# Kernel optimization log

Measured on AMD Instinct MI355X. Metric: run time of the kernel, lower is better.

## Reference

```python
import jax, jax.numpy as jnp
import numpy as np

B, S, D = 16, 2048, 64
K, M = 8, 2048

def setup_inputs() -> dict:
    key = jax.random.key(0)
    kx, kc = jax.random.split(key)
    x = jax.random.normal(kx, (B, S, D), dtype=jnp.float32)
    # nn.init.uniform_(weight, -1/M, 1/M)
    codebooks = jax.random.uniform(kc, (K, M, D), dtype=jnp.float32,
                                   minval=-1.0 / M, maxval=1.0 / M)
    return {"x": x, "codebooks": codebooks}

def reference(x, codebooks):
    """Residual VQ: sequentially quantize residual against K codebooks.

    x: (B,S,D) float32; codebooks: (K,M,D) float32.
    Returns (quantized (B,S,D), indices (K,B,S) int32).
    Uses squared-distance expansion ||r||^2 - 2 r.c + ||c||^2 (argmin-equivalent
    to torch.norm) to avoid materializing the (B,S,M,D) difference tensor.
    """
    def step(residual, cb):  # residual: (B,S,D), cb: (M,D)
        r2 = jnp.sum(residual * residual, axis=-1, keepdims=True)   # (B,S,1)
        c2 = jnp.sum(cb * cb, axis=-1)                              # (M,)
        cross = jnp.einsum('bsd,md->bsm', residual, cb)             # (B,S,M)
        d2 = r2 - 2.0 * cross + c2                                  # (B,S,M)
        idx = jnp.argmin(d2, axis=-1)                               # (B,S)
        q = cb[idx]                                                 # (B,S,D) gather
        return residual - q, idx

    residual, indices = jax.lax.scan(step, x, codebooks)
    quantized = x - residual
    return quantized, indices
```

## Files before the change

### kernel.cpp

```cpp
#include <hip/hip_runtime.h>


#define BB 16
#define SS 2048
#define DD 64
#define KK 8
#define MM 2048
#define NPTS (BB * SS)
#define QSIZE (NPTS * DD)
#define WPB 8
#define MCHUNK (MM / WPB)

__global__ __launch_bounds__(256) void rvq_prep(const float* __restrict__ cb,
                                                float* __restrict__ c2) {
#pragma clang fp contract(off)
    int tid = blockIdx.x * 256 + threadIdx.x;
    const float* row = cb + (size_t)tid * DD;
    float r[8];
#pragma unroll
    for (int j = 0; j < 8; ++j) { float v = row[j]; r[j] = v * v; }
#pragma unroll
    for (int i = 8; i < DD; i += 8) {
#pragma unroll
        for (int j = 0; j < 8; ++j) { float v = row[i + j]; float t = v * v; r[j] += t; }
    }
    c2[tid] = ((r[0] + r[1]) + (r[2] + r[3])) + ((r[4] + r[5]) + (r[6] + r[7]));
}

#define R2G(a0,a1,a2,a3,a4,a5,a6,a7) \
    "v_mul_f32 v96, v" a0 ", v" a0 "\n\tv_add_f32 v80, v80, v96\n\t" \
    "v_mul_f32 v96, v" a1 ", v" a1 "\n\tv_add_f32 v81, v81, v96\n\t" \
    "v_mul_f32 v96, v" a2 ", v" a2 "\n\tv_add_f32 v82, v82, v96\n\t" \
    "v_mul_f32 v96, v" a3 ", v" a3 "\n\tv_add_f32 v83, v83, v96\n\t" \
    "v_mul_f32 v96, v" a4 ", v" a4 "\n\tv_add_f32 v84, v84, v96\n\t" \
    "v_mul_f32 v96, v" a5 ", v" a5 "\n\tv_add_f32 v85, v85, v96\n\t" \
    "v_mul_f32 v96, v" a6 ", v" a6 "\n\tv_add_f32 v86, v86, v96\n\t" \
    "v_mul_f32 v96, v" a7 ", v" a7 "\n\tv_add_f32 v87, v87, v96\n\t"

#define FQ(s0,s1,s2,s3,w0,w1,w2,w3) \
    "v_fma_f32 v81, s" s0 ", v" w0 ", v81\n\t" \
    "v_fma_f32 v82, s" s1 ", v" w1 ", v82\n\t" \
    "v_fma_f32 v83, s" s2 ", v" w2 ", v83\n\t" \
    "v_fma_f32 v84, s" s3 ", v" w3 ", v84\n\t"

__global__ __launch_bounds__(512, 4) void rvq_step(const float* __restrict__ res_in,
                                                   float* __restrict__ res_out,
                                                   const float* __restrict__ cbk,
                                                   const float* __restrict__ c2k,
                                                   float* __restrict__ idx_out) {
#pragma clang fp contract(off)
    const int tid = threadIdx.x;
    const int lane = tid & 63;
    const int wv = __builtin_amdgcn_readfirstlane(tid >> 6);
    const int point = blockIdx.x * 64 + lane;
    const int m0 = wv * MCHUNK;
    const float* cbw = cbk + (size_t)m0 * DD;
    const float* c2w = c2k + m0;
    const unsigned long long ra = (unsigned long long)(res_in + (size_t)point * DD);

    unsigned mk0, mk1, mk2, mk3, mk4, mk5, mk6, mk7;
    asm volatile(
        "global_load_dwordx4 v[16:19], %[ra], off\n\t"
        "global_load_dwordx4 v[20:23], %[ra], off offset:16\n\t"
        "global_load_dwordx4 v[24:27], %[ra], off offset:32\n\t"
        "global_load_dwordx4 v[28:31], %[ra], off offset:48\n\t"
        "global_load_dwordx4 v[32:35], %[ra], off offset:64\n\t"
        "global_load_dwordx4 v[36:39], %[ra], off offset:80\n\t"
        "global_load_dwordx4 v[40:43], %[ra], off offset:96\n\t"
        "global_load_dwordx4 v[44:47], %[ra], off offset:112\n\t"
        "global_load_dwordx4 v[48:51], %[ra], off offset:128\n\t"
        "global_load_dwordx4 v[52:55], %[ra], off offset:144\n\t"
        "global_load_dwordx4 v[56:59], %[ra], off offset:160\n\t"
        "global_load_dwordx4 v[60:63], %[ra], off offset:176\n\t"
        "global_load_dwordx4 v[64:67], %[ra], off offset:192\n\t"
        "global_load_dwordx4 v[68:71], %[ra], off offset:208\n\t"
        "global_load_dwordx4 v[72:75], %[ra], off offset:224\n\t"
        "global_load_dwordx4 v[76:79], %[ra], off offset:240\n\t"
        "s_waitcnt vmcnt(0)\n\t"
        "v_mul_f32 v80, v16, v16\n\t"
        "v_mul_f32 v81, v17, v17\n\t"
        "v_mul_f32 v82, v18, v18\n\t"
        "v_mul_f32 v83, v19, v19\n\t"
        "v_mul_f32 v84, v20, v20\n\t"
        "v_mul_f32 v85, v21, v21\n\t"
        "v_mul_f32 v86, v22, v22\n\t"
        "v_mul_f32 v87, v23, v23\n\t"
        R2G("24","25","26","27","28","29","30","31")
        R2G("32","33","34","35","36","37","38","39")
        R2G("40","41","42","43","44","45","46","47")
        R2G("48","49","50","51","52","53","54","55")
        R2G("56","57","58","59","60","61","62","63")
        R2G("64","65","66","67","68","69","70","71")
        R2G("72","73","74","75","76","77","78","79")
        "v_add_f32 v96, v80, v81\n\t"
        "v_add_f32 v97, v82, v83\n\t"
        "v_add_f32 v96, v96, v97\n\t"
        "v_add_f32 v97, v84, v85\n\t"
        "v_add_f32 v80, v86, v87\n\t"
        "v_add_f32 v97, v97, v80\n\t"
        "v_add_f32 v80, v96, v97\n\t"
        "v_mov_b32 v85, 0x7f800000\n\t"
        "v_mov_b32 v86, 1\n\t"
        "v_mov_b32 v87, 0\n\t"
        "v_mov_b32 v88, 0\n\t"
        "v_mov_b32 v89, 0\n\t"
        "v_mov_b32 v90, 0\n\t"
        "v_mov_b32 v91, 0\n\t"
        "v_mov_b32 v92, 0\n\t"
        "v_mov_b32 v93, 0\n\t"
        "v_mov_b32 v94, 0\n\t"
        "v_mov_b32 v95, 0\n\t"
        "s_mov_b32 s29, 0\n\t"
        "s_mov_b32 s25, 8\n\t"
        "Lout_%=:\n\t"
        "s_mov_b32 s24, 32\n\t"
        "Linn_%=:\n\t"
        "s_load_dwordx16 s[32:47], %[cb], s29\n\t"
        "s_add_u32 s30, s29, 64\n\t"
        "s_load_dwordx16 s[48:63], %[cb], s30\n\t"
        "s_add_u32 s30, s29, 128\n\t"
        "s_load_dwordx16 s[64:79], %[cb], s30\n\t"
        "s_add_u32 s30, s29, 192\n\t"
        "s_load_dwordx16 s[80:95], %[cb], s30\n\t"
        "s_lshr_b32 s31, s29, 6\n\t"
        "s_load_dword s28, %[c2], s31\n\t"
        "s_add_u32 s29, s29, 256\n\t"
        "s_waitcnt lgkmcnt(0)\n\t"
        "v_mul_f32 v81, s32, v16\n\t"
        "v_mul_f32 v82, s33, v17\n\t"
        "v_mul_f32 v83, s34, v18\n\t"
        "v_mul_f32 v84, s35, v19\n\t"
        FQ("36","37","38","39","20","21","22","23")
        FQ("40","41","42","43","24","25","26","27")
        FQ("44","45","46","47","28","29","30","31")
        FQ("48","49","50","51","32","33","34","35")
        FQ("52","53","54","55","36","37","38","39")
        FQ("56","57","58","59","40","41","42","43")
        FQ("60","61","62","63","44","45","46","47")
        FQ("64","65","66","67","48","49","50","51")
        FQ("68","69","70","71","52","53","54","55")
        FQ("72","73","74","75","56","57","58","59")
        FQ("76","77","78","79","60","61","62","63")
        FQ("80","81","82","83","64","65","66","67")
        FQ("84","85","86","87","68","69","70","71")
        FQ("88","89","90","91","72","73","74","75")
        FQ("92","93","94","95","76","77","78","79")
        "v_add_f32 v96, v81, v82\n\t"
        "v_add_f32 v97, v83, v84\n\t"
        "v_add_f32 v96, v96, v97\n\t"
        "v_fma_f32 v96, v96, -2.0, v80\n\t"
        "v_add_f32 v96, s28, v96\n\t"
        "v_add_f32 v97, %[mg], v85\n\t"
        "v_cmp_lt_f32 vcc, v96, v97\n\t"
        "v_cndmask_b32 v97, 0, v86, vcc\n\t"
        "v_or_b32 v87, v87, v97\n\t"
        "v_min_f32 v85, v85, v96\n\t"
        "v_lshlrev_b32 v86, 1, v86\n\t"
        "s_sub_u32 s24, s24, 1\n\t"
        "s_cmp_lg_u32 s24, 0\n\t"
        "s_cbranch_scc1 Linn_%=\n\t"
        "v_mov_b32 v88, v89\n\t"
        "v_mov_b32 v89, v90\n\t"
        "v_mov_b32 v90, v91\n\t"
        "v_mov_b32 v91, v92\n\t"
        "v_mov_b32 v92, v93\n\t"
        "v_mov_b32 v93, v94\n\t"
        "v_mov_b32 v94, v95\n\t"
        "v_mov_b32 v95, v87\n\t"
        "v_mov_b32 v87, 0\n\t"
        "v_mov_b32 v86, 1\n\t"
        "s_sub_u32 s25, s25, 1\n\t"
        "s_cmp_lg_u32 s25, 0\n\t"
        "s_cbranch_scc1 Lout_%=\n\t"
        "v_mov_b32 %[o0], v88\n\t"
        "v_mov_b32 %[o1], v89\n\t"
        "v_mov_b32 %[o2], v90\n\t"
        "v_mov_b32 %[o3], v91\n\t"
        "v_mov_b32 %[o4], v92\n\t"
        "v_mov_b32 %[o5], v93\n\t"
        "v_mov_b32 %[o6], v94\n\t"
        "v_mov_b32 %[o7], v95\n\t"
        : [o0] "=v"(mk0), [o1] "=v"(mk1), [o2] "=v"(mk2), [o3] "=v"(mk3),
          [o4] "=v"(mk4), [o5] "=v"(mk5), [o6] "=v"(mk6), [o7] "=v"(mk7)
        : [ra] "v"(ra), [cb] "s"(cbw), [c2] "s"(c2w), [mg] "s"(2.0e-4f)
        : "vcc", "scc",
          "v16","v17","v18","v19","v20","v21","v22","v23","v24","v25","v26","v27",
          "v28","v29","v30","v31","v32","v33","v34","v35","v36","v37","v38","v39",
          "v40","v41","v42","v43","v44","v45","v46","v47","v48","v49","v50","v51",
          "v52","v53","v54","v55","v56","v57","v58","v59","v60","v61","v62","v63",
          "v64","v65","v66","v67","v68","v69","v70","v71","v72","v73","v74","v75",
          "v76","v77","v78","v79","v80","v81","v82","v83","v84","v85","v86","v87",
          "v88","v89","v90","v91","v92","v93","v94","v95","v96","v97",
          "s24","s25","s28","s29","s30","s31",
          "s32","s33","s34","s35","s36","s37","s38","s39",
          "s40","s41","s42","s43","s44","s45","s46","s47","s48","s49","s50","s51",
          "s52","s53","s54","s55","s56","s57","s58","s59","s60","s61","s62","s63",
          "s64","s65","s66","s67","s68","s69","s70","s71","s72","s73","s74","s75",
          "s76","s77","s78","s79","s80","s81","s82","s83","s84","s85","s86","s87",
          "s88","s89","s90","s91","s92","s93","s94","s95");

    const unsigned mk[8] = {mk0, mk1, mk2, mk3, mk4, mk5, mk6, mk7};
    const float* rr = res_in + (size_t)point * DD;
    float rv[DD];
#pragma unroll
    for (int i = 0; i < DD / 4; ++i) {
        float4 v = ((const float4*)rr)[i];
        rv[4 * i] = v.x; rv[4 * i + 1] = v.y; rv[4 * i + 2] = v.z; rv[4 * i + 3] = v.w;
    }
    float r8[8];
#pragma unroll
    for (int j = 0; j < 8; ++j) r8[j] = rv[j] * rv[j];
#pragma unroll
    for (int i = 8; i < DD; i += 8) {
#pragma unroll
        for (int j = 0; j < 8; ++j) { float t = rv[i + j] * rv[i + j]; r8[j] += t; }
    }
    const float r2e = ((r8[0] + r8[1]) + (r8[2] + r8[3])) + ((r8[4] + r8[5]) + (r8[6] + r8[7]));

    float beste = __builtin_inff();
    int bide = m0;
    for (int g = 0; g < 8; ++g) {
        unsigned mask = mk[g];
        while (mask) {
            const int bit = __builtin_ctz(mask);
            mask &= mask - 1;
            const int m = m0 + g * 32 + bit;
            const float4* crow4 = (const float4*)(cbk + (size_t)m * DD);
            float ch[4] = {0.0f, 0.0f, 0.0f, 0.0f};
#pragma unroll
            for (int b = 0; b < DD; b += 16) {
                float cw[16], rw[16];
#pragma unroll
                for (int q = 0; q < 4; ++q) {
                    float4 cv = crow4[(b >> 2) + q];
                    cw[4 * q] = cv.x; cw[4 * q + 1] = cv.y; cw[4 * q + 2] = cv.z; cw[4 * q + 3] = cv.w;
                    rw[4 * q] = rv[b + 4 * q]; rw[4 * q + 1] = rv[b + 4 * q + 1];
                    rw[4 * q + 2] = rv[b + 4 * q + 2]; rw[4 * q + 3] = rv[b + 4 * q + 3];
                }
#pragma unroll
                for (int gg = 3; gg >= 0; --gg) {
#pragma unroll
                    for (int j = 0; j < 4; ++j) {
                        const int d = gg * 4 + j;
                        float tp = rw[d] * cw[d];
                        ch[j] += tp;
                    }
                }
            }
            const float cross = (ch[0] + ch[1]) + (ch[2] + ch[3]);
            const float tt = __builtin_fmaf(-2.0f, cross, r2e);
            const float d2 = tt + c2k[m];
            if (d2 < beste) { beste = d2; bide = m; }
        }
    }

    __shared__ float sb[WPB * 64];
    __shared__ int   si[WPB * 64];
    __shared__ int   fidx[64];
    sb[wv * 64 + lane] = beste;
    si[wv * 64 + lane] = bide;
    __syncthreads();
    if (tid < 64) {
        float b = sb[lane];
        int ix = si[lane];
#pragma unroll
        for (int w = 1; w < WPB; ++w) {
            float ob = sb[w * 64 + lane];
            int oi = si[w * 64 + lane];
            if (ob < b) { b = ob; ix = oi; }
        }
        fidx[lane] = ix;
        idx_out[point] = (float)ix;
    }
    __syncthreads();

    const size_t base = (size_t)blockIdx.x * 64 * DD;
#pragma unroll
    for (int i = 0; i < 8; ++i) {
        const int e = i * 512 + tid;
        const int p = e >> 6;
        const int d = e & 63;
        const int ix = fidx[p];
        res_out[base + e] = res_in[base + e] - cbk[(size_t)ix * DD + d];
    }
}

__global__ __launch_bounds__(256) void rvq_final(const float* __restrict__ x,
                                                 const float* __restrict__ res,
                                                 float* __restrict__ q) {
#pragma clang fp contract(off)
    int i = blockIdx.x * 256 + threadIdx.x;
    q[i] = x[i] - res[i];
}

extern "C" void kernel_launch(void* const* d_in, const int* in_sizes, int n_in,
                              void* d_out, int out_size, void* d_ws, size_t ws_size,
                              hipStream_t stream) {
    const float* x  = (const float*)d_in[0];
    const float* cb = (const float*)d_in[1];

    float* out = (float*)d_out;
    float* quant = out;
    float* idx_out = out + QSIZE;

    float* c2   = (float*)d_ws;
    float* res1 = c2 + (size_t)KK * MM;
    float* R[2] = { quant, res1 };

    rvq_prep<<<(KK * MM) / 256, 256, 0, stream>>>(cb, c2);

    for (int k = 0; k < KK; ++k) {
        const float* rin = (k == 0) ? x : R[(k - 1) & 1];
        float* rout = R[k & 1];
        rvq_step<<<NPTS / 64, 512, 0, stream>>>(
            rin, rout,
            cb + (size_t)k * MM * DD,
            c2 + (size_t)k * MM,
            idx_out + (size_t)k * NPTS);
    }

    rvq_final<<<QSIZE / 256, 256, 0, stream>>>(x, R[(KK - 1) & 1], quant);
}
```

Before: 1.554 ms.

## Move exact candidate rescoring pass into inline assembly and tighten margin

The second pass, which rescores candidate codewords flagged by the fast first-pass masks with exact fp32 arithmetic, moves from compiled C++ into the same inline-asm block. It reuses the residual already held in registers instead of reloading it, and emits the best distance and index directly rather than returning eight mask registers. The candidate margin is halved from 2e-4 to 1e-4, so fewer candidates are rescored, at some risk of missing the true argmin when the first-pass error exceeds the margin. The asm issues a blocking wait for every codeword load, so load latency is not hidden.

```diff
diff --git a/kernel.cpp b/kernel.cpp
--- a/kernel.cpp
+++ b/kernel.cpp
@@ -42,6 +42,69 @@
     "v_fma_f32 v82, s" s1 ", v" w1 ", v82\n\t" \
     "v_fma_f32 v83, s" s2 ", v" w2 ", v83\n\t" \
     "v_fma_f32 v84, s" s3 ", v" w3 ", v84\n\t"
+
+#define XA(c, r, ch) \
+    "v_mul_f32 v116, v" c ", v" r "\n\tv_add_f32 v" ch ", v" ch ", v116\n\t"
+#define XI(c, r, ch) \
+    "v_mul_f32 v" ch ", v" c ", v" r "\n\t"
+
+#define QADDR(QOFFADD) \
+    "v_lshlrev_b32 v97, 8, v96\n\t" \
+    QOFFADD \
+    "v_mov_b32 v115, %[cbh]\n\t" \
+    "v_add_co_u32 v114, vcc, %[cbl], v97\n\t" \
+    "v_addc_co_u32 v115, vcc, 0, v115, vcc\n\t" \
+    "global_load_dwordx4 v[98:101], v[114:115], off\n\t" \
+    "global_load_dwordx4 v[102:105], v[114:115], off offset:16\n\t" \
+    "global_load_dwordx4 v[106:109], v[114:115], off offset:32\n\t" \
+    "global_load_dwordx4 v[110:113], v[114:115], off offset:48\n\t" \
+    "s_waitcnt vmcnt(0)\n\t"
+
+#define QCONS(r12,r13,r14,r15, r8,r9,r10,r11, r4,r5,r6,r7, r0,r1,r2,r3, G3A) \
+    G3A("110", r12, "81") G3A("111", r13, "82") G3A("112", r14, "83") G3A("113", r15, "84") \
+    XA("106", r8,  "81") XA("107", r9,  "82") XA("108", r10, "83") XA("109", r11, "84") \
+    XA("102", r4,  "81") XA("103", r5,  "82") XA("104", r6,  "83") XA("105", r7,  "84") \
+    XA("98",  r0,  "81") XA("99",  r1,  "82") XA("100", r2,  "83") XA("101", r3,  "84")
+
+#define PASS2G(G, MR, ORBIT) \
+    "Lh" G "_%=:\n\t" \
+    "v_cmp_ne_u32 vcc, 0, v" MR "\n\t" \
+    "s_cbranch_vccz Le" G "_%=\n\t" \
+    "s_mov_b64 s[22:23], vcc\n\t" \
+    "v_ffbl_b32 v96, v" MR "\n\t" \
+    "v_and_b32 v96, 31, v96\n\t" \
+    "v_add_u32 v97, -1, v" MR "\n\t" \
+    "v_and_b32 v" MR ", v" MR ", v97\n\t" \
+    ORBIT \
+     \
+    QADDR("") \
+    QCONS("28","29","30","31","24","25","26","27","20","21","22","23","16","17","18","19", XI) \
+    QADDR("v_add_u32 v97, 64, v97\n\t") \
+    QCONS("44","45","46","47","40","41","42","43","36","37","38","39","32","33","34","35", XA) \
+    QADDR("v_add_u32 v97, 0x80, v97\n\t") \
+    QCONS("60","61","62","63","56","57","58","59","52","53","54","55","48","49","50","51", XA) \
+    QADDR("v_add_u32 v97, 0xc0, v97\n\t") \
+    QCONS("76","77","78","79","72","73","74","75","68","69","70","71","64","65","66","67", XA) \
+     \
+    "v_add_f32 v97, v81, v82\n\t" \
+    "v_add_f32 v116, v83, v84\n\t" \
+    "v_add_f32 v97, v97, v116\n\t" \
+    "v_fma_f32 v97, v97, -2.0, v80\n\t" \
+    "v_lshlrev_b32 v114, 2, v96\n\t" \
+    "v_mov_b32 v115, %[c2h]\n\t" \
+    "v_add_co_u32 v114, vcc, %[c2l], v114\n\t" \
+    "v_addc_co_u32 v115, vcc, 0, v115, vcc\n\t" \
+    "global_load_dword v116, v[114:115], off\n\t" \
+    "s_waitcnt vmcnt(0)\n\t" \
+    "v_add_f32 v97, v116, v97\n\t" \
+     \
+    "v_cmp_lt_f32 vcc, v97, v85\n\t" \
+    "s_and_b64 vcc, vcc, s[22:23]\n\t" \
+    "v_cndmask_b32 v85, v85, v97, vcc\n\t" \
+    "v_add_u32 v116, %[m0], v96\n\t" \
+    "v_cndmask_b32 v86, v86, v116, vcc\n\t" \
+    "s_branch Lh" G "_%=\n\t" \
+    "Le" G "_%=:\n\t"
 
 __global__ __launch_bounds__(512, 4) void rvq_step(const float* __restrict__ res_in,
                                                    float* __restrict__ res_out,
@@ -57,8 +120,13 @@
     const float* cbw = cbk + (size_t)m0 * DD;
     const float* c2w = c2k + m0;
     const unsigned long long ra = (unsigned long long)(res_in + (size_t)point * DD);
-
-    unsigned mk0, mk1, mk2, mk3, mk4, mk5, mk6, mk7;
+    const unsigned cbl = (unsigned)(unsigned long long)cbw;
+    const unsigned cbh = (unsigned)(((unsigned long long)cbw) >> 32);
+    const unsigned c2l = (unsigned)(unsigned long long)c2w;
+    const unsigned c2h = (unsigned)(((unsigned long long)c2w) >> 32);
+
+    float best;
+    int bidx;
     asm volatile(
         "global_load_dwordx4 v[16:19], %[ra], off\n\t"
         "global_load_dwordx4 v[20:23], %[ra], off offset:16\n\t"
@@ -172,17 +240,22 @@
         "s_sub_u32 s25, s25, 1\n\t"
         "s_cmp_lg_u32 s25, 0\n\t"
         "s_cbranch_scc1 Lout_%=\n\t"
-        "v_mov_b32 %[o0], v88\n\t"
-        "v_mov_b32 %[o1], v89\n\t"
-        "v_mov_b32 %[o2], v90\n\t"
-        "v_mov_b32 %[o3], v91\n\t"
-        "v_mov_b32 %[o4], v92\n\t"
-        "v_mov_b32 %[o5], v93\n\t"
-        "v_mov_b32 %[o6], v94\n\t"
-        "v_mov_b32 %[o7], v95\n\t"
-        : [o0] "=v"(mk0), [o1] "=v"(mk1), [o2] "=v"(mk2), [o3] "=v"(mk3),
-          [o4] "=v"(mk4), [o5] "=v"(mk5), [o6] "=v"(mk6), [o7] "=v"(mk7)
-        : [ra] "v"(ra), [cb] "s"(cbw), [c2] "s"(c2w), [mg] "s"(2.0e-4f)
+        "v_mov_b32 v85, 0x7f800000\n\t"
+        "v_mov_b32 v86, 0\n\t"
+        PASS2G("0", "88", "")
+        PASS2G("1", "89", "v_or_b32 v96, 32, v96\n\t")
+        PASS2G("2", "90", "v_or_b32 v96, 64, v96\n\t")
+        PASS2G("3", "91", "v_or_b32 v96, 0x60, v96\n\t")
+        PASS2G("4", "92", "v_or_b32 v96, 0x80, v96\n\t")
+        PASS2G("5", "93", "v_or_b32 v96, 0xa0, v96\n\t")
+        PASS2G("6", "94", "v_or_b32 v96, 0xc0, v96\n\t")
+        PASS2G("7", "95", "v_or_b32 v96, 0xe0, v96\n\t")
+        "v_mov_b32 %[ob], v85\n\t"
+        "v_mov_b32 %[oi], v86\n\t"
+        : [ob] "=v"(best), [oi] "=v"(bidx)
+        : [ra] "v"(ra), [cb] "s"(cbw), [c2] "s"(c2w), [m0] "s"(m0),
+          [mg] "s"(1.0e-4f), [cbl] "s"(cbl), [cbh] "s"(cbh),
+          [c2l] "s"(c2l), [c2h] "s"(c2h)
         : "vcc", "scc",
           "v16","v17","v18","v19","v20","v21","v22","v23","v24","v25","v26","v27",
           "v28","v29","v30","v31","v32","v33","v34","v35","v36","v37","v38","v39",
@@ -190,8 +263,10 @@
           "v52","v53","v54","v55","v56","v57","v58","v59","v60","v61","v62","v63",
           "v64","v65","v66","v67","v68","v69","v70","v71","v72","v73","v74","v75",
           "v76","v77","v78","v79","v80","v81","v82","v83","v84","v85","v86","v87",
-          "v88","v89","v90","v91","v92","v93","v94","v95","v96","v97",
-          "s24","s25","s28","s29","s30","s31",
+          "v88","v89","v90","v91","v92","v93","v94","v95","v96","v97","v98","v99",
+          "v100","v101","v102","v103","v104","v105","v106","v107","v108","v109",
+          "v110","v111","v112","v113","v114","v115","v116",
+          "s22","s23","s24","s25","s28","s29","s30","s31",
           "s32","s33","s34","s35","s36","s37","s38","s39",
           "s40","s41","s42","s43","s44","s45","s46","s47","s48","s49","s50","s51",
           "s52","s53","s54","s55","s56","s57","s58","s59","s60","s61","s62","s63",
@@ -199,66 +274,11 @@
           "s76","s77","s78","s79","s80","s81","s82","s83","s84","s85","s86","s87",
           "s88","s89","s90","s91","s92","s93","s94","s95");
 
-    const unsigned mk[8] = {mk0, mk1, mk2, mk3, mk4, mk5, mk6, mk7};
-    const float* rr = res_in + (size_t)point * DD;
-    float rv[DD];
-#pragma unroll
-    for (int i = 0; i < DD / 4; ++i) {
-        float4 v = ((const float4*)rr)[i];
-        rv[4 * i] = v.x; rv[4 * i + 1] = v.y; rv[4 * i + 2] = v.z; rv[4 * i + 3] = v.w;
-    }
-    float r8[8];
-#pragma unroll
-    for (int j = 0; j < 8; ++j) r8[j] = rv[j] * rv[j];
-#pragma unroll
-    for (int i = 8; i < DD; i += 8) {
-#pragma unroll
-        for (int j = 0; j < 8; ++j) { float t = rv[i + j] * rv[i + j]; r8[j] += t; }
-    }
-    const float r2e = ((r8[0] + r8[1]) + (r8[2] + r8[3])) + ((r8[4] + r8[5]) + (r8[6] + r8[7]));
-
-    float beste = __builtin_inff();
-    int bide = m0;
-    for (int g = 0; g < 8; ++g) {
-        unsigned mask = mk[g];
-        while (mask) {
-            const int bit = __builtin_ctz(mask);
-            mask &= mask - 1;
-            const int m = m0 + g * 32 + bit;
-            const float4* crow4 = (const float4*)(cbk + (size_t)m * DD);
-            float ch[4] = {0.0f, 0.0f, 0.0f, 0.0f};
-#pragma unroll
-            for (int b = 0; b < DD; b += 16) {
-                float cw[16], rw[16];
-#pragma unroll
-                for (int q = 0; q < 4; ++q) {
-                    float4 cv = crow4[(b >> 2) + q];
-                    cw[4 * q] = cv.x; cw[4 * q + 1] = cv.y; cw[4 * q + 2] = cv.z; cw[4 * q + 3] = cv.w;
-                    rw[4 * q] = rv[b + 4 * q]; rw[4 * q + 1] = rv[b + 4 * q + 1];
-                    rw[4 * q + 2] = rv[b + 4 * q + 2]; rw[4 * q + 3] = rv[b + 4 * q + 3];
-                }
-#pragma unroll
-                for (int gg = 3; gg >= 0; --gg) {
-#pragma unroll
-                    for (int j = 0; j < 4; ++j) {
-                        const int d = gg * 4 + j;
-                        float tp = rw[d] * cw[d];
-                        ch[j] += tp;
-                    }
-                }
-            }
-            const float cross = (ch[0] + ch[1]) + (ch[2] + ch[3]);
-            const float tt = __builtin_fmaf(-2.0f, cross, r2e);
-            const float d2 = tt + c2k[m];
-            if (d2 < beste) { beste = d2; bide = m; }
-        }
-    }
-
     __shared__ float sb[WPB * 64];
     __shared__ int   si[WPB * 64];
     __shared__ int   fidx[64];
-    sb[wv * 64 + lane] = beste;
-    si[wv * 64 + lane] = bide;
+    sb[wv * 64 + lane] = best;
+    si[wv * 64 + lane] = bidx;
     __syncthreads();
     if (tid < 64) {
         float b = sb[lane];
```

Result: no change. 1.547 ms (-0.5%).
